# Optimization experiments

Hardware: AMD Instinct MI355X
Metric: run time of the kernel (lower is better)

## Reference

```python
import math
import jax, jax.numpy as jnp
import numpy as np

N_HEAD = 16
LORA_SCALE = 16.0 / 8.0  # lora_alpha / r


def lora_linear(x, W, b, A, B):
    # y = x @ W^T + b + scale * (x @ A^T) @ B^T
    base = jnp.einsum('btc,oc->bto', x, W) + b
    low = jnp.einsum('btc,rc->btr', x, A)
    return base + LORA_SCALE * jnp.einsum('btr,or->bto', low, B)


def setup_inputs() -> dict:
    key = jax.random.key(0)
    ks = jax.random.split(key, 8)
    B, T, C = 2, 2048, 1024
    r = 8
    s = 0.02
    return {
        'x': jax.random.normal(ks[0], (B, T, C), jnp.float32),
        'W_attn': jax.random.normal(ks[1], (3 * C, C), jnp.float32) * s,
        'b_attn': jnp.zeros((3 * C,), jnp.float32),
        'A_attn': jax.random.normal(ks[2], (r, C), jnp.float32) * s,
        'B_attn': jax.random.normal(ks[3], (3 * C, r), jnp.float32) * s,
        'W_proj': jax.random.normal(ks[4], (C, C), jnp.float32) * s,
        'b_proj': jnp.zeros((C,), jnp.float32),
        'A_proj': jax.random.normal(ks[5], (r, C), jnp.float32) * s,
        'B_proj': jax.random.normal(ks[6], (C, r), jnp.float32) * s,
    }


def reference(x, W_attn, b_attn, A_attn, B_attn, W_proj, b_proj, A_proj, B_proj):
    B, T, C = x.shape
    H = N_HEAD
    hd = C // H
    qkv = lora_linear(x, W_attn, b_attn, A_attn, B_attn)  # [B,T,3C]
    q, k, v = jnp.split(qkv, 3, axis=2)
    # [B,H,T,hd]
    q = q.reshape(B, T, H, hd).transpose(0, 2, 1, 3)
    k = k.reshape(B, T, H, hd).transpose(0, 2, 1, 3)
    v = v.reshape(B, T, H, hd).transpose(0, 2, 1, 3)
    att = jnp.einsum('bhqd,bhkd->bhqk', q, k) * (1.0 / math.sqrt(hd))
    causal = jnp.tril(jnp.ones((T, T), bool))
    att = jnp.where(causal, att, -jnp.inf)
    att = jax.nn.softmax(att, axis=-1)
    out = jnp.einsum('bhqk,bhkd->bhqd', att, v)
    out = out.transpose(0, 2, 1, 3).reshape(B, T, C)
    return lora_linear(out, W_proj, b_proj, A_proj, B_proj)
```

## Files before the change

kernel.cpp:

```cpp
#include <hip/hip_runtime.h>
#include <hip/hip_bf16.h>
#include <stdint.h>

typedef __bf16 bf16_t;
typedef __bf16 bf16x8 __attribute__((ext_vector_type(8)));
typedef __bf16 bf16x4 __attribute__((ext_vector_type(4)));
typedef __bf16 bf16x2 __attribute__((ext_vector_type(2)));
typedef float f32x4 __attribute__((ext_vector_type(4)));
typedef float f32x16 __attribute__((ext_vector_type(16)));
typedef uint32_t u32;
typedef uint32_t u32x4 __attribute__((ext_vector_type(4)));

typedef __attribute__((address_space(1))) void as1void;
typedef __attribute__((address_space(3))) void as3void;

#define LOG2E 1.44269504088896340736f

__device__ __forceinline__ void gll16(const void* g, void* l) {
  __builtin_amdgcn_global_load_lds((as1void*)g, (as3void*)l, 16, 0, 0);
}

__device__ __forceinline__ u32 pack2(float a, float b) {
  bf16x2 t = {(bf16_t)a, (bf16_t)b};
  return __builtin_bit_cast(u32, t);
}

__global__ void prep_weff2(const float* __restrict__ W_attn, const float* __restrict__ B_attn,
                           const float* __restrict__ A_attn, const float* __restrict__ W_proj,
                           const float* __restrict__ B_proj, const float* __restrict__ A_proj,
                           bf16_t* __restrict__ WaE, bf16_t* __restrict__ WpE) {
  int idx = blockIdx.x * 256 + threadIdx.x;
  const float *W, *Bm, *Am;
  bf16_t* dst;
  if (idx < 3145728) {
    W = W_attn; Bm = B_attn; Am = A_attn; dst = WaE;
  } else {
    idx -= 3145728;
    W = W_proj; Bm = B_proj; Am = A_proj; dst = WpE;
  }
  int o = idx >> 10, c = idx & 1023;
  float acc = W[idx];
#pragma unroll
  for (int r = 0; r < 8; ++r)
    acc += 2.0f * Bm[o * 8 + r] * Am[r * 1024 + c];
  dst[idx] = (bf16_t)acc;
}

__global__ void cast_bf4(const float4* __restrict__ X, bf16x4* __restrict__ Xb, int n4) {
  int i = blockIdx.x * 256 + threadIdx.x;
  if (i < n4) {
    float4 v = X[i];
    bf16x4 o = {(bf16_t)v.x, (bf16_t)v.y, (bf16_t)v.z, (bf16_t)v.w};
    Xb[i] = o;
  }
}

template <bool QKV>
__global__ __launch_bounds__(256, 3) void gemm_bt(
    const bf16_t* __restrict__ A, const bf16_t* __restrict__ Bt,
    const float* __restrict__ bias,
    bf16_t* __restrict__ Qb, bf16_t* __restrict__ Kb, bf16_t* __restrict__ Vb,
    float* __restrict__ Out) {
  __shared__ bf16_t Als[128][64];
  __shared__ bf16_t Bls[128][64];
  const int m0 = blockIdx.x * 128;
  const int n0 = blockIdx.y * 128;
  const int tid = threadIdx.x;
  const int lane = tid & 63;
  const int w = tid >> 6;
  const int wm = w >> 1, wn = w & 1;
  const int lr = lane & 15, g = lane >> 4;
  const int sw = (lane & 7) << 3;
  const int srow = lane >> 3;
  const int soff = ((lane & 7) ^ srow) * 8;

  f32x4 acc[4][4] = {};

  for (int k0 = 0; k0 < 1024; k0 += 64) {
#pragma unroll
    for (int c = 0; c < 4; ++c) {
      int r = w * 32 + c * 8 + srow;
      gll16(A + (size_t)(m0 + r) * 1024 + k0 + soff, &Als[w * 32 + c * 8][0]);
      gll16(Bt + (size_t)(n0 + r) * 1024 + k0 + soff, &Bls[w * 32 + c * 8][0]);
    }
    __syncthreads();
#pragma unroll
    for (int ks = 0; ks < 2; ++ks) {
      bf16x8 af[4], bfv[4];
#pragma unroll
      for (int i = 0; i < 4; ++i)
        af[i] = *(const bf16x8*)&Als[wm * 64 + i * 16 + lr][(ks * 32 + g * 8) ^ sw];
#pragma unroll
      for (int j = 0; j < 4; ++j)
        bfv[j] = *(const bf16x8*)&Bls[wn * 64 + j * 16 + lr][(ks * 32 + g * 8) ^ sw];
#pragma unroll
      for (int i = 0; i < 4; ++i)
#pragma unroll
        for (int j = 0; j < 4; ++j)
          acc[i][j] = __builtin_amdgcn_mfma_f32_16x16x32_bf16(af[i], bfv[j], acc[i][j], 0, 0, 0);
    }
    __syncthreads();
  }

#pragma unroll
  for (int i = 0; i < 4; ++i) {
#pragma unroll
    for (int j = 0; j < 4; ++j) {
#pragma unroll
      for (int e = 0; e < 4; ++e) {
        int m = m0 + wm * 64 + i * 16 + g * 4 + e;
        int n = n0 + wn * 64 + j * 16 + lr;
        float v = acc[i][j][e] + bias[n];
        if (QKV) {
          int b = m >> 11, t = m & 2047;
          int which = n >> 10, hn = n & 1023;
          int h = hn >> 6, d = hn & 63;
          bf16_t* dst = (which == 0) ? Qb : (which == 1) ? Kb : Vb;
          dst[(((size_t)(b * 16 + h)) * 2048 + t) * 64 + d] = (bf16_t)v;
        } else {
          Out[(size_t)m * 1024 + n] = v;
        }
      }
    }
  }
}

__global__ __launch_bounds__(256, 2) void attn_fwd(
    const bf16_t* __restrict__ Qb, const bf16_t* __restrict__ Kb,
    const bf16_t* __restrict__ Vb, bf16_t* __restrict__ Ob) {
  __shared__ bf16_t Kls[2][128][64];
  __shared__ bf16_t Vt[2][64][128];

  int id = blockIdx.x;
  int xcd = id & 7, j = id >> 3;
  int lo = j & 31, hi2 = j >> 5;
  int bh = xcd * 4 + (lo & 3);
  int qb = hi2 ? 15 - (lo >> 2) : (lo >> 2);
  int b = bh >> 4, h = bh & 15;

  const int tid = threadIdx.x, lane = tid & 63, w = tid >> 6;
  const int q32 = lane & 31;
  const int hi = lane >> 5;
  const int ksw = (q32 & 7) << 3;
  const int vkey = ((q32 & 7) ^ (q32 >> 2)) << 3;
  const bf16_t* Qp = Qb + (size_t)bh * 2048 * 64;
  const bf16_t* Kp = Kb + (size_t)bh * 2048 * 64;
  const bf16_t* Vp = Vb + (size_t)bh * 2048 * 64;
  const float sc = 0.125f * LOG2E;

  const int q0 = qb * 128;
  const int qrow = q0 + w * 32 + q32;

  const int kbase = (tid >> 4) * 8;
  const int dbase = (tid & 15) * 4;
  const int ksr = lane >> 3;
  const int kso = ((lane & 7) ^ ksr) * 8;

  bf16x8 qf[4];
#pragma unroll
  for (int ds = 0; ds < 4; ++ds)
    qf[ds] = *(const bf16x8*)(Qp + (size_t)qrow * 64 + ds * 16 + hi * 8);

  float m_run = -3e38f, l_run = 0.f;
  f32x16 o_acc[2] = {};
  const int ktiles = qb + 1;

  {
    uint2 rowv[8];
#pragma unroll
    for (int r = 0; r < 8; ++r)
      rowv[r] = *(const uint2*)(Vp + (size_t)(kbase + r) * 64 + dbase);
#pragma unroll
    for (int c = 0; c < 4; ++c) {
      int rb = w * 32 + c * 8;
      gll16(Kp + (size_t)(rb + ksr) * 64 + kso, &Kls[0][rb][0]);
    }
#pragma unroll
    for (int dd = 0; dd < 4; ++dd) {
      u32 sel = (dd & 1) ? 0x07060302u : 0x05040100u;
      u32 a0 = (dd >> 1) ? rowv[0].y : rowv[0].x;
      u32 a1 = (dd >> 1) ? rowv[1].y : rowv[1].x;
      u32 a2 = (dd >> 1) ? rowv[2].y : rowv[2].x;
      u32 a3 = (dd >> 1) ? rowv[3].y : rowv[3].x;
      u32 a4 = (dd >> 1) ? rowv[4].y : rowv[4].x;
      u32 a5 = (dd >> 1) ? rowv[5].y : rowv[5].x;
      u32 a6 = (dd >> 1) ? rowv[6].y : rowv[6].x;
      u32 a7 = (dd >> 1) ? rowv[7].y : rowv[7].x;
      int4 val;
      val.x = __builtin_amdgcn_perm(a1, a0, sel);
      val.y = __builtin_amdgcn_perm(a3, a2, sel);
      val.z = __builtin_amdgcn_perm(a5, a4, sel);
      val.w = __builtin_amdgcn_perm(a7, a6, sel);
      int d = dbase + dd;
      int key = ((d & 7) ^ ((d >> 2) & 7)) << 3;
      *(int4*)&Vt[0][d][kbase ^ key] = val;
    }
    __syncthreads();
  }

  int cb = 0;
  for (int kt = 0; kt < ktiles; ++kt) {
    const bool lastt = (kt == ktiles - 1);
    const int nfa = lastt ? (w + 1) : 4;
    const int k0 = kt * 128;
    const int nb = cb ^ 1;

    uint2 rowv[8];
    if (!lastt) {
      const int kn = k0 + 128;
#pragma unroll
      for (int r = 0; r < 8; ++r)
        rowv[r] = *(const uint2*)(Vp + (size_t)(kn + kbase + r) * 64 + dbase);
#pragma unroll
      for (int c = 0; c < 4; ++c) {
        int rb = w * 32 + c * 8;
        gll16(Kp + (size_t)(kn + rb + ksr) * 64 + kso, &Kls[nb][rb][0]);
      }
    }

    f32x16 s[4] = {};
#pragma unroll
    for (int fa = 0; fa < 4; ++fa) {
      if (fa < nfa) {
#pragma unroll
        for (int ds = 0; ds < 4; ++ds) {
          bf16x8 kf = *(const bf16x8*)&Kls[cb][fa * 32 + q32][(ds * 16 + hi * 8) ^ ksw];
          s[fa] = __builtin_amdgcn_mfma_f32_32x32x16_bf16(kf, qf[ds], s[fa], 0, 0, 0);
        }
      }
    }

    float mloc = -3e38f;
#pragma unroll
    for (int fa = 0; fa < 4; ++fa) {
      if (fa < nfa) {
#pragma unroll
        for (int r = 0; r < 16; ++r) {
          float v = s[fa][r] * sc;
          if (lastt && fa == w) {
            int km = (r & 3) + 8 * (r >> 2) + 4 * hi;
            if (km > q32) v = -3e38f;
          }
          s[fa][r] = v;
          mloc = fmaxf(mloc, v);
        }
      }
    }
    mloc = fmaxf(mloc, __shfl_xor(mloc, 32, 64));
    if (!__all(mloc <= m_run + 8.0f)) {
      float mnew = fmaxf(m_run, mloc);
      float rs = __builtin_amdgcn_exp2f(m_run - mnew);
      m_run = mnew;
      l_run *= rs;
      o_acc[0] *= rs;
      o_acc[1] *= rs;
    }

    if (!lastt) {
#pragma unroll
      for (int dd = 0; dd < 4; ++dd) {
        u32 sel = (dd & 1) ? 0x07060302u : 0x05040100u;
        u32 a0 = (dd >> 1) ? rowv[0].y : rowv[0].x;
        u32 a1 = (dd >> 1) ? rowv[1].y : rowv[1].x;
        u32 a2 = (dd >> 1) ? rowv[2].y : rowv[2].x;
        u32 a3 = (dd >> 1) ? rowv[3].y : rowv[3].x;
        u32 a4 = (dd >> 1) ? rowv[4].y : rowv[4].x;
        u32 a5 = (dd >> 1) ? rowv[5].y : rowv[5].x;
        u32 a6 = (dd >> 1) ? rowv[6].y : rowv[6].x;
        u32 a7 = (dd >> 1) ? rowv[7].y : rowv[7].x;
        int4 val;
        val.x = __builtin_amdgcn_perm(a1, a0, sel);
        val.y = __builtin_amdgcn_perm(a3, a2, sel);
        val.z = __builtin_amdgcn_perm(a5, a4, sel);
        val.w = __builtin_amdgcn_perm(a7, a6, sel);
        int d = dbase + dd;
        int key = ((d & 7) ^ ((d >> 2) & 7)) << 3;
        *(int4*)&Vt[nb][d][kbase ^ key] = val;
      }
    }

    float lsum = 0.f;
#pragma unroll
    for (int fa = 0; fa < 4; ++fa) {
      if (fa < nfa) {
        float p[16];
#pragma unroll
        for (int r = 0; r < 16; ++r) {
          p[r] = __builtin_amdgcn_exp2f(s[fa][r] - m_run);
          lsum += p[r];
        }
        u32 x0 = pack2(p[0], p[1]),   x1 = pack2(p[2], p[3]);
        u32 x2 = pack2(p[4], p[5]),   x3 = pack2(p[6], p[7]);
        u32 y0 = pack2(p[8], p[9]),   y1 = pack2(p[10], p[11]);
        u32 y2 = pack2(p[12], p[13]), y3 = pack2(p[14], p[15]);
        u32 z0 = hi ? x0 : x2;
        u32 z1 = hi ? x1 : x3;
        u32 z2 = hi ? y0 : y2;
        u32 z3 = hi ? y1 : y3;
        z0 = (u32)__shfl_xor((int)z0, 32, 64);
        z1 = (u32)__shfl_xor((int)z1, 32, 64);
        z2 = (u32)__shfl_xor((int)z2, 32, 64);
        z3 = (u32)__shfl_xor((int)z3, 32, 64);
        u32x4 pw0 = hi ? (u32x4){z0, z1, x2, x3} : (u32x4){x0, x1, z0, z1};
        u32x4 pw1 = hi ? (u32x4){z2, z3, y2, y3} : (u32x4){y0, y1, z2, z3};
        bf16x8 P0 = __builtin_bit_cast(bf16x8, pw0);
        bf16x8 P1 = __builtin_bit_cast(bf16x8, pw1);
#pragma unroll
        for (int db = 0; db < 2; ++db) {
          int d = db * 32 + q32;
          bf16x8 vf0 = *(const bf16x8*)&Vt[cb][d][(fa * 32 + hi * 8) ^ vkey];
          o_acc[db] = __builtin_amdgcn_mfma_f32_32x32x16_bf16(vf0, P0, o_acc[db], 0, 0, 0);
          bf16x8 vf1 = *(const bf16x8*)&Vt[cb][d][(fa * 32 + 16 + hi * 8) ^ vkey];
          o_acc[db] = __builtin_amdgcn_mfma_f32_32x32x16_bf16(vf1, P1, o_acc[db], 0, 0, 0);
        }
      }
    }
    lsum += __shfl_xor(lsum, 32, 64);
    l_run += lsum;

    __syncthreads();
    cb = nb;
  }

  float inv = 1.0f / l_run;
  bf16_t* obase = Ob + ((size_t)(b * 2048 + qrow)) * 1024 + h * 64;
#pragma unroll
  for (int db = 0; db < 2; ++db) {
#pragma unroll
    for (int rg = 0; rg < 4; ++rg) {
      bf16x4 ov = {(bf16_t)(o_acc[db][rg * 4 + 0] * inv),
                   (bf16_t)(o_acc[db][rg * 4 + 1] * inv),
                   (bf16_t)(o_acc[db][rg * 4 + 2] * inv),
                   (bf16_t)(o_acc[db][rg * 4 + 3] * inv)};
      *(bf16x4*)(obase + db * 32 + rg * 8 + hi * 4) = ov;
    }
  }
}

extern "C" void kernel_launch(void* const* d_in, const int* in_sizes, int n_in,
                              void* d_out, int out_size, void* d_ws, size_t ws_size,
                              hipStream_t stream) {
  const float* x      = (const float*)d_in[0];
  const float* W_attn = (const float*)d_in[1];
  const float* b_attn = (const float*)d_in[2];
  const float* A_attn = (const float*)d_in[3];
  const float* B_attn = (const float*)d_in[4];
  const float* W_proj = (const float*)d_in[5];
  const float* b_proj = (const float*)d_in[6];
  const float* A_proj = (const float*)d_in[7];
  const float* B_proj = (const float*)d_in[8];
  float* out = (float*)d_out;

  char* ws = (char*)d_ws;
  bf16_t* WaE = (bf16_t*)(ws);
  bf16_t* WpE = (bf16_t*)(ws + 6291456);
  bf16_t* Xb  = (bf16_t*)(ws + 8388608);
  bf16_t* Qb  = (bf16_t*)(ws + 16777216);
  bf16_t* Kb  = (bf16_t*)(ws + 25165824);
  bf16_t* Vb  = (bf16_t*)(ws + 33554432);
  bf16_t* Ob  = (bf16_t*)(ws + 41943040);

  prep_weff2<<<16384, 256, 0, stream>>>(W_attn, B_attn, A_attn, W_proj, B_proj, A_proj, WaE, WpE);
  cast_bf4<<<4096, 256, 0, stream>>>((const float4*)x, (bf16x4*)Xb, 1048576);

  gemm_bt<true><<<dim3(32, 24), 256, 0, stream>>>(Xb, WaE, b_attn, Qb, Kb, Vb, nullptr);
  attn_fwd<<<512, 256, 0, stream>>>(Qb, Kb, Vb, Ob);
  gemm_bt<false><<<dim3(32, 8), 256, 0, stream>>>(Ob, WpE, b_proj, nullptr, nullptr, nullptr, out);
}
```

Before: 112.4 us.

## Fuse prep kernels, fold softmax scale into Q, single-buffer K with setprio

Merges the weight-folding and x-cast kernels into one launch to save a launch. Folds the 1/sqrt(hd)*log2e scale into Q inside the QKV GEMM epilogue, removing a per-score multiply in attention. Single-buffers K in LDS, restructured so QK^T runs first and is followed by a barrier before the next K prefetch. This frees LDS for three blocks per CU, and s_setprio hints are added around the MFMA sections. Also simplifies the V-transpose swizzle keys; the reduced K buffering may expose load latency.

```diff
diff --git a/kernel.cpp b/kernel.cpp
--- a/kernel.cpp
+++ b/kernel.cpp
@@ -15,6 +15,7 @@
 typedef __attribute__((address_space(3))) void as3void;
 
 #define LOG2E 1.44269504088896340736f
+#define QSCALE 0.18033688011112042f
 
 __device__ __forceinline__ void gll16(const void* g, void* l) {
   __builtin_amdgcn_global_load_lds((as1void*)g, (as3void*)l, 16, 0, 0);
@@ -25,31 +26,32 @@
   return __builtin_bit_cast(u32, t);
 }
 
-__global__ void prep_weff2(const float* __restrict__ W_attn, const float* __restrict__ B_attn,
-                           const float* __restrict__ A_attn, const float* __restrict__ W_proj,
-                           const float* __restrict__ B_proj, const float* __restrict__ A_proj,
-                           bf16_t* __restrict__ WaE, bf16_t* __restrict__ WpE) {
-  int idx = blockIdx.x * 256 + threadIdx.x;
-  const float *W, *Bm, *Am;
-  bf16_t* dst;
-  if (idx < 3145728) {
-    W = W_attn; Bm = B_attn; Am = A_attn; dst = WaE;
+__global__ void prep_all(const float* __restrict__ W_attn, const float* __restrict__ B_attn,
+                         const float* __restrict__ A_attn, const float* __restrict__ W_proj,
+                         const float* __restrict__ B_proj, const float* __restrict__ A_proj,
+                         const float4* __restrict__ x,
+                         bf16_t* __restrict__ WaE, bf16_t* __restrict__ WpE,
+                         bf16x4* __restrict__ Xb) {
+  int bid = blockIdx.x;
+  if (bid < 16384) {
+    int idx = bid * 256 + threadIdx.x;
+    const float *W, *Bm, *Am;
+    bf16_t* dst;
+    if (idx < 3145728) {
+      W = W_attn; Bm = B_attn; Am = A_attn; dst = WaE;
+    } else {
+      idx -= 3145728;
+      W = W_proj; Bm = B_proj; Am = A_proj; dst = WpE;
+    }
+    int o = idx >> 10, c = idx & 1023;
+    float acc = W[idx];
+#pragma unroll
+    for (int r = 0; r < 8; ++r)
+      acc += 2.0f * Bm[o * 8 + r] * Am[r * 1024 + c];
+    dst[idx] = (bf16_t)acc;
   } else {
-    idx -= 3145728;
-    W = W_proj; Bm = B_proj; Am = A_proj; dst = WpE;
-  }
-  int o = idx >> 10, c = idx & 1023;
-  float acc = W[idx];
-#pragma unroll
-  for (int r = 0; r < 8; ++r)
-    acc += 2.0f * Bm[o * 8 + r] * Am[r * 1024 + c];
-  dst[idx] = (bf16_t)acc;
-}
-
-__global__ void cast_bf4(const float4* __restrict__ X, bf16x4* __restrict__ Xb, int n4) {
-  int i = blockIdx.x * 256 + threadIdx.x;
-  if (i < n4) {
-    float4 v = X[i];
+    int i = (bid - 16384) * 256 + threadIdx.x;
+    float4 v = x[i];
     bf16x4 o = {(bf16_t)v.x, (bf16_t)v.y, (bf16_t)v.z, (bf16_t)v.w};
     Xb[i] = o;
   }
@@ -115,6 +117,7 @@
           int b = m >> 11, t = m & 2047;
           int which = n >> 10, hn = n & 1023;
           int h = hn >> 6, d = hn & 63;
+          if (which == 0) v *= QSCALE;
           bf16_t* dst = (which == 0) ? Qb : (which == 1) ? Kb : Vb;
           dst[(((size_t)(b * 16 + h)) * 2048 + t) * 64 + d] = (bf16_t)v;
         } else {
@@ -125,10 +128,10 @@
   }
 }
 
-__global__ __launch_bounds__(256, 2) void attn_fwd(
+__global__ __launch_bounds__(256, 3) void attn_fwd(
     const bf16_t* __restrict__ Qb, const bf16_t* __restrict__ Kb,
     const bf16_t* __restrict__ Vb, bf16_t* __restrict__ Ob) {
-  __shared__ bf16_t Kls[2][128][64];
+  __shared__ bf16_t Kls[128][64];
   __shared__ bf16_t Vt[2][64][128];
 
   int id = blockIdx.x;
@@ -142,17 +145,17 @@
   const int q32 = lane & 31;
   const int hi = lane >> 5;
   const int ksw = (q32 & 7) << 3;
-  const int vkey = ((q32 & 7) ^ (q32 >> 2)) << 3;
+  const int vkey = (q32 >> 2) << 3;
   const bf16_t* Qp = Qb + (size_t)bh * 2048 * 64;
   const bf16_t* Kp = Kb + (size_t)bh * 2048 * 64;
   const bf16_t* Vp = Vb + (size_t)bh * 2048 * 64;
-  const float sc = 0.125f * LOG2E;
 
   const int q0 = qb * 128;
   const int qrow = q0 + w * 32 + q32;
 
   const int kbase = (tid >> 4) * 8;
   const int dbase = (tid & 15) * 4;
+  const int wkey = ((tid & 15) & 7) << 3;
   const int ksr = lane >> 3;
   const int kso = ((lane & 7) ^ ksr) * 8;
 
@@ -166,15 +169,15 @@
   const int ktiles = qb + 1;
 
   {
+#pragma unroll
+    for (int c = 0; c < 4; ++c) {
+      int rb = w * 32 + c * 8;
+      gll16(Kp + (size_t)(rb + ksr) * 64 + kso, &Kls[rb][0]);
+    }
     uint2 rowv[8];
 #pragma unroll
     for (int r = 0; r < 8; ++r)
       rowv[r] = *(const uint2*)(Vp + (size_t)(kbase + r) * 64 + dbase);
-#pragma unroll
-    for (int c = 0; c < 4; ++c) {
-      int rb = w * 32 + c * 8;
-      gll16(Kp + (size_t)(rb + ksr) * 64 + kso, &Kls[0][rb][0]);
-    }
 #pragma unroll
     for (int dd = 0; dd < 4; ++dd) {
       u32 sel = (dd & 1) ? 0x07060302u : 0x05040100u;
@@ -191,9 +194,7 @@
       val.y = __builtin_amdgcn_perm(a3, a2, sel);
       val.z = __builtin_amdgcn_perm(a5, a4, sel);
       val.w = __builtin_amdgcn_perm(a7, a6, sel);
-      int d = dbase + dd;
-      int key = ((d & 7) ^ ((d >> 2) & 7)) << 3;
-      *(int4*)&Vt[0][d][kbase ^ key] = val;
+      *(int4*)&Vt[0][dbase + dd][kbase ^ wkey] = val;
     }
     __syncthreads();
   }
@@ -202,48 +203,49 @@
   for (int kt = 0; kt < ktiles; ++kt) {
     const bool lastt = (kt == ktiles - 1);
     const int nfa = lastt ? (w + 1) : 4;
-    const int k0 = kt * 128;
     const int nb = cb ^ 1;
+
+    f32x16 s[4] = {};
+    __builtin_amdgcn_s_setprio(1);
+#pragma unroll
+    for (int fa = 0; fa < 4; ++fa) {
+      if (fa < nfa) {
+#pragma unroll
+        for (int ds = 0; ds < 4; ++ds) {
+          bf16x8 kf = *(const bf16x8*)&Kls[fa * 32 + q32][(ds * 16 + hi * 8) ^ ksw];
+          s[fa] = __builtin_amdgcn_mfma_f32_32x32x16_bf16(kf, qf[ds], s[fa], 0, 0, 0);
+        }
+      }
+    }
+    __builtin_amdgcn_s_setprio(0);
+    __syncthreads();
 
     uint2 rowv[8];
     if (!lastt) {
-      const int kn = k0 + 128;
+      const int kn = (kt + 1) * 128;
+#pragma unroll
+      for (int c = 0; c < 4; ++c) {
+        int rb = w * 32 + c * 8;
+        gll16(Kp + (size_t)(kn + rb + ksr) * 64 + kso, &Kls[rb][0]);
+      }
 #pragma unroll
       for (int r = 0; r < 8; ++r)
         rowv[r] = *(const uint2*)(Vp + (size_t)(kn + kbase + r) * 64 + dbase);
-#pragma unroll
-      for (int c = 0; c < 4; ++c) {
-        int rb = w * 32 + c * 8;
-        gll16(Kp + (size_t)(kn + rb + ksr) * 64 + kso, &Kls[nb][rb][0]);
-      }
-    }
-
-    f32x16 s[4] = {};
+    }
+
+    float mloc = -3e38f;
 #pragma unroll
     for (int fa = 0; fa < 4; ++fa) {
       if (fa < nfa) {
-#pragma unroll
-        for (int ds = 0; ds < 4; ++ds) {
-          bf16x8 kf = *(const bf16x8*)&Kls[cb][fa * 32 + q32][(ds * 16 + hi * 8) ^ ksw];
-          s[fa] = __builtin_amdgcn_mfma_f32_32x32x16_bf16(kf, qf[ds], s[fa], 0, 0, 0);
-        }
-      }
-    }
-
-    float mloc = -3e38f;
-#pragma unroll
-    for (int fa = 0; fa < 4; ++fa) {
-      if (fa < nfa) {
-#pragma unroll
-        for (int r = 0; r < 16; ++r) {
-          float v = s[fa][r] * sc;
-          if (lastt && fa == w) {
+        if (lastt && fa == w) {
+#pragma unroll
+          for (int r = 0; r < 16; ++r) {
             int km = (r & 3) + 8 * (r >> 2) + 4 * hi;
-            if (km > q32) v = -3e38f;
+            if (km > q32) s[fa][r] = -3e38f;
           }
-          s[fa][r] = v;
-          mloc = fmaxf(mloc, v);
-        }
+        }
+#pragma unroll
+        for (int r = 0; r < 16; ++r) mloc = fmaxf(mloc, s[fa][r]);
       }
     }
     mloc = fmaxf(mloc, __shfl_xor(mloc, 32, 64));
@@ -273,9 +275,7 @@
         val.y = __builtin_amdgcn_perm(a3, a2, sel);
         val.z = __builtin_amdgcn_perm(a5, a4, sel);
         val.w = __builtin_amdgcn_perm(a7, a6, sel);
-        int d = dbase + dd;
-        int key = ((d & 7) ^ ((d >> 2) & 7)) << 3;
-        *(int4*)&Vt[nb][d][kbase ^ key] = val;
+        *(int4*)&Vt[nb][dbase + dd][kbase ^ wkey] = val;
       }
     }
 
@@ -305,6 +305,7 @@
         u32x4 pw1 = hi ? (u32x4){z2, z3, y2, y3} : (u32x4){y0, y1, z2, z3};
         bf16x8 P0 = __builtin_bit_cast(bf16x8, pw0);
         bf16x8 P1 = __builtin_bit_cast(bf16x8, pw1);
+        __builtin_amdgcn_s_setprio(1);
 #pragma unroll
         for (int db = 0; db < 2; ++db) {
           int d = db * 32 + q32;
@@ -313,6 +314,7 @@
           bf16x8 vf1 = *(const bf16x8*)&Vt[cb][d][(fa * 32 + 16 + hi * 8) ^ vkey];
           o_acc[db] = __builtin_amdgcn_mfma_f32_32x32x16_bf16(vf1, P1, o_acc[db], 0, 0, 0);
         }
+        __builtin_amdgcn_s_setprio(0);
       }
     }
     lsum += __shfl_xor(lsum, 32, 64);
@@ -360,8 +362,8 @@
   bf16_t* Vb  = (bf16_t*)(ws + 33554432);
   bf16_t* Ob  = (bf16_t*)(ws + 41943040);
 
-  prep_weff2<<<16384, 256, 0, stream>>>(W_attn, B_attn, A_attn, W_proj, B_proj, A_proj, WaE, WpE);
-  cast_bf4<<<4096, 256, 0, stream>>>((const float4*)x, (bf16x4*)Xb, 1048576);
+  prep_all<<<20480, 256, 0, stream>>>(W_attn, B_attn, A_attn, W_proj, B_proj, A_proj,
+                                      (const float4*)x, WaE, WpE, (bf16x4*)Xb);
 
   gemm_bt<true><<<dim3(32, 24), 256, 0, stream>>>(Xb, WaE, b_attn, Qb, Kb, Vb, nullptr);
   attn_fwd<<<512, 256, 0, stream>>>(Qb, Kb, Vb, Ob);
```

Result: slower. 118.6 us (+5.5%).
